# Performance work log

Hardware: AMD Instinct MI355X
Metric: run time of the kernel (lower is better)

Reference implementation:

```python
import jax, jax.numpy as jnp
import numpy as np

N = 50000      # num nodes
EG = 1600000   # num edges (avg degree 32)
IN = 64        # in_dim
OUT = 64       # out_dim
H = 4          # num_heads
D = OUT // H   # per-head dim


def setup_inputs() -> dict:
    key = jax.random.key(0)
    ks = jax.random.split(key, 12)
    s = 1.0 / np.sqrt(IN)
    return {
        "x": jax.random.normal(ks[0], (N, IN), jnp.float32),
        "edge_attr": jax.random.normal(ks[1], (EG, IN), jnp.float32),
        "edge_index": jax.random.randint(ks[2], (2, EG), 0, N, jnp.int32),
        "Wq": jax.random.uniform(ks[3], (OUT, IN), jnp.float32, -s, s),
        "bq": jax.random.uniform(ks[4], (OUT,), jnp.float32, -s, s),
        "Wk": jax.random.uniform(ks[5], (OUT, IN), jnp.float32, -s, s),
        "bk": jax.random.uniform(ks[6], (OUT,), jnp.float32, -s, s),
        "We": jax.random.uniform(ks[7], (OUT, IN), jnp.float32, -s, s),
        "be": jax.random.uniform(ks[8], (OUT,), jnp.float32, -s, s),
        "Wv": jax.random.uniform(ks[9], (OUT, IN), jnp.float32, -s, s),
        "bv": jax.random.uniform(ks[10], (OUT,), jnp.float32, -s, s),
    }


def reference(x, edge_attr, edge_index, Wq, bq, Wk, bk, We, be, Wv, bv):
    n = x.shape[0]
    # linear projections, reshaped to [*, H, D]
    Qh = (x @ Wq.T + bq).reshape(n, H, D)
    Kh = (x @ Wk.T + bk).reshape(n, H, D)
    Vh = (x @ Wv.T + bv).reshape(n, H, D)
    Ee = (edge_attr @ We.T + be).reshape(-1, H, D)
    src = edge_index[0]
    dst = edge_index[1]
    # per-edge score: sum_d K[src] * Q[dst] / sqrt(D) * E  -> [E, H]
    score = ((Kh[src] * Qh[dst]) * (1.0 / np.sqrt(D)) * Ee).sum(-1)
    score = jnp.exp(jnp.clip(score, -5.0, 5.0))            # [E, H]
    msg = Vh[src] * score[..., None]                        # [E, H, D]
    wV = jax.ops.segment_sum(msg, dst, num_segments=n)      # [N, H, D]
    # note: original forward returns wV without dividing by Z
    return wV.reshape(n, H * D)
```

## Files before the change

### kernel.cpp

```cpp
#include <hip/hip_runtime.h>


typedef __attribute__((ext_vector_type(8))) short bf16x8;
typedef __attribute__((ext_vector_type(4))) float f32x4;

union frag_u { uint32_t u[4]; uint4 u4; bf16x8 v; };

__device__ __forceinline__ uint32_t pack2(float a, float b) {
    return (__float_as_uint(a) >> 16) | (__float_as_uint(b) & 0xffff0000u);
}

__device__ __forceinline__ void cvt4(float4 v, uint32_t& h0, uint32_t& h1,
                                     uint32_t& l0, uint32_t& l1) {
    float hx = __uint_as_float(__float_as_uint(v.x) & 0xffff0000u);
    float hy = __uint_as_float(__float_as_uint(v.y) & 0xffff0000u);
    float hz = __uint_as_float(__float_as_uint(v.z) & 0xffff0000u);
    float hw = __uint_as_float(__float_as_uint(v.w) & 0xffff0000u);
    h0 = pack2(v.x, v.y);
    h1 = pack2(v.z, v.w);
    l0 = pack2(v.x - hx, v.y - hy);
    l1 = pack2(v.z - hz, v.w - hw);
}

__global__ __launch_bounds__(256) void proj_kernel(
    const float* __restrict__ x,
    const float* __restrict__ Wq, const float* __restrict__ bq,
    const float* __restrict__ Wk, const float* __restrict__ bk,
    const float* __restrict__ Wv, const float* __restrict__ bv,
    float* __restrict__ Qb, float* __restrict__ KV,
    int n)
{
    __shared__ float WqT[64 * 65];
    __shared__ float WkT[64 * 65];
    __shared__ float WvT[64 * 65];
    __shared__ float xs[4][4][64];

    const int tid  = threadIdx.x;
    const int wave = tid >> 6;
    const int lane = tid & 63;

    #pragma unroll
    for (int k = 0; k < 16; ++k) {
        int idx = tid + k * 256;
        int j = idx >> 6, i = idx & 63;
        WqT[i * 65 + j] = Wq[idx];
        WkT[i * 65 + j] = Wk[idx];
        WvT[i * 65 + j] = Wv[idx];
    }
    const float bqv = bq[lane];
    const float bkv = bk[lane];
    const float bvv = bv[lane];
    __syncthreads();

    for (int blockbase = blockIdx.x * 16; blockbase < n;
         blockbase += gridDim.x * 16) {
        int base = blockbase + wave * 4;
        #pragma unroll
        for (int j = 0; j < 4; ++j) {
            int node = base + j;
            xs[wave][j][lane] = (node < n) ? x[node * 64 + lane] : 0.f;
        }
        __syncthreads();

        float accq[4], acck[4], accv[4];
        #pragma unroll
        for (int j = 0; j < 4; ++j) { accq[j] = bqv; acck[j] = bkv; accv[j] = bvv; }

        #pragma unroll
        for (int f = 0; f < 16; ++f) {
            float wq[4], wk[4], wv[4];
            #pragma unroll
            for (int u = 0; u < 4; ++u) {
                int i = 4 * f + u;
                wq[u] = WqT[i * 65 + lane];
                wk[u] = WkT[i * 65 + lane];
                wv[u] = WvT[i * 65 + lane];
            }
            #pragma unroll
            for (int j = 0; j < 4; ++j) {
                float4 xv = *reinterpret_cast<const float4*>(&xs[wave][j][4 * f]);
                accq[j] = fmaf(xv.x, wq[0], accq[j]);
                accq[j] = fmaf(xv.y, wq[1], accq[j]);
                accq[j] = fmaf(xv.z, wq[2], accq[j]);
                accq[j] = fmaf(xv.w, wq[3], accq[j]);
                acck[j] = fmaf(xv.x, wk[0], acck[j]);
                acck[j] = fmaf(xv.y, wk[1], acck[j]);
                acck[j] = fmaf(xv.z, wk[2], acck[j]);
                acck[j] = fmaf(xv.w, wk[3], acck[j]);
                accv[j] = fmaf(xv.x, wv[0], accv[j]);
                accv[j] = fmaf(xv.y, wv[1], accv[j]);
                accv[j] = fmaf(xv.z, wv[2], accv[j]);
                accv[j] = fmaf(xv.w, wv[3], accv[j]);
            }
        }

        #pragma unroll
        for (int j = 0; j < 4; ++j) {
            int node = base + j;
            if (node < n) {
                Qb[(size_t)node * 64 + lane]       = accq[j];
                KV[(size_t)node * 128 + lane]      = acck[j];
                KV[(size_t)node * 128 + 64 + lane] = accv[j];
            }
        }
        __syncthreads();
    }
}

__global__ __launch_bounds__(256) void edge_kernel(
    const float* __restrict__ ea, const int* __restrict__ ei,
    const float* __restrict__ Qb, const float* __restrict__ KV,
    const float* __restrict__ We, const float* __restrict__ be,
    float* __restrict__ out, int EG)
{
    __shared__ uint4 bfragLDS[16][64];

    const int tid  = threadIdx.x;
    const int wave = __builtin_amdgcn_readfirstlane(tid >> 6);
    const int lane = tid & 63;
    const int g    = lane >> 4;
    const int q    = lane & 15;

    {
        const int nt = wave;
        #pragma unroll
        for (int ks = 0; ks < 2; ++ks) {
            frag_u fh, fl;
            #pragma unroll
            for (int b = 0; b < 2; ++b) {
                float4 w4 = *reinterpret_cast<const float4*>(
                    &We[(size_t)(16 * nt + q) * 64 + 32 * ks + 16 * b + 4 * g]);
                cvt4(w4, fh.u[2 * b + 0], fh.u[2 * b + 1],
                         fl.u[2 * b + 0], fl.u[2 * b + 1]);
            }
            bfragLDS[nt * 4 + ks * 2 + 0][lane] = fh.u4;
            bfragLDS[nt * 4 + ks * 2 + 1][lane] = fl.u4;
        }
    }
    float bias4[4];
    #pragma unroll
    for (int nt = 0; nt < 4; ++nt) bias4[nt] = be[16 * nt + q];
    __syncthreads();

    const int nw  = gridDim.x * 4;
    const int wid = blockIdx.x * 4 + wave;

    for (int eb = wid * 16; eb < EG; eb += nw * 16) {
        int srcs[16], dsts[16];
        #pragma unroll
        for (int r = 0; r < 16; ++r) {
            srcs[r] = ei[eb + r];
            dsts[r] = ei[EG + eb + r];
        }

        frag_u Ah[2], Al[2];
        const float* arow = &ea[(size_t)(eb + q) * 64];
        #pragma unroll
        for (int ks = 0; ks < 2; ++ks) {
            #pragma unroll
            for (int b = 0; b < 2; ++b) {
                float4 a4 = *reinterpret_cast<const float4*>(
                    &arow[32 * ks + 16 * b + 4 * g]);
                cvt4(a4, Ah[ks].u[2 * b + 0], Ah[ks].u[2 * b + 1],
                         Al[ks].u[2 * b + 0], Al[ks].u[2 * b + 1]);
            }
        }

        f32x4 acc[4];
        #pragma unroll
        for (int nt = 0; nt < 4; ++nt) {
            acc[nt][0] = bias4[nt]; acc[nt][1] = bias4[nt];
            acc[nt][2] = bias4[nt]; acc[nt][3] = bias4[nt];
            #pragma unroll
            for (int ks = 0; ks < 2; ++ks) {
                frag_u bh, bl;
                bh.u4 = bfragLDS[nt * 4 + ks * 2 + 0][lane];
                bl.u4 = bfragLDS[nt * 4 + ks * 2 + 1][lane];
                acc[nt] = __builtin_amdgcn_mfma_f32_16x16x32_bf16(
                              Al[ks].v, bh.v, acc[nt], 0, 0, 0);
                acc[nt] = __builtin_amdgcn_mfma_f32_16x16x32_bf16(
                              Ah[ks].v, bl.v, acc[nt], 0, 0, 0);
                acc[nt] = __builtin_amdgcn_mfma_f32_16x16x32_bf16(
                              Ah[ks].v, bh.v, acc[nt], 0, 0, 0);
            }
        }

        #pragma unroll
        for (int r = 0; r < 4; ++r) {
            const int snid = (g & 2) ? ((g & 1) ? srcs[12 + r] : srcs[8 + r])
                                     : ((g & 1) ? srcs[4 + r]  : srcs[r]);
            const int dnid = (g & 2) ? ((g & 1) ? dsts[12 + r] : dsts[8 + r])
                                     : ((g & 1) ? dsts[4 + r]  : dsts[r]);
            const float* kb = KV + (size_t)snid * 128 + q;
            const float* qp = Qb + (size_t)dnid * 64 + q;
            float*       ob = out + (size_t)dnid * 64 + q;

            #pragma unroll
            for (int nt = 0; nt < 4; ++nt) {
                const float kv = kb[16 * nt];
                const float qv = qp[16 * nt];
                float t = kv * qv * 0.25f * acc[nt][r];
                t += __shfl_xor(t, 1);
                t += __shfl_xor(t, 2);
                t += __shfl_xor(t, 4);
                t += __shfl_xor(t, 8);
                t = fminf(fmaxf(t, -5.f), 5.f);
                const float s  = __expf(t);
                const float vv = kb[64 + 16 * nt];
                atomicAdd(&ob[16 * nt], vv * s);
            }
        }
    }
}

extern "C" void kernel_launch(void* const* d_in, const int* in_sizes, int n_in,
                              void* d_out, int out_size, void* d_ws, size_t ws_size,
                              hipStream_t stream) {
    const float* x   = (const float*)d_in[0];
    const float* ea  = (const float*)d_in[1];
    const int*   ei  = (const int*)d_in[2];
    const float* Wq  = (const float*)d_in[3];
    const float* bq  = (const float*)d_in[4];
    const float* Wk  = (const float*)d_in[5];
    const float* bk  = (const float*)d_in[6];
    const float* We  = (const float*)d_in[7];
    const float* be  = (const float*)d_in[8];
    const float* Wv  = (const float*)d_in[9];
    const float* bv  = (const float*)d_in[10];
    float* out = (float*)d_out;

    const int n  = in_sizes[0] / 64;
    const int EG = in_sizes[1] / 64;

    float* Qb = (float*)d_ws;
    float* KV = Qb + (size_t)n * 64;

    hipMemsetAsync(d_out, 0, (size_t)out_size * sizeof(float), stream);

    const int projGrid = (n + 15) / 16;
    proj_kernel<<<projGrid, 256, 0, stream>>>(x, Wq, bq, Wk, bk, Wv, bv,
                                              Qb, KV, n);

    edge_kernel<<<2500, 256, 0, stream>>>(ea, ei, Qb, KV, We, be, out, EG);
}
```

Measured before the change: 546.5 us.

## Replace atomic scatter with CSR-by-destination aggregation via count, scan, permute

Builds a destination-sorted CSR (degree histogram fused into the projection kernel, three-pass scan, atomic scatter into a permutation) and then aggregates per destination node in registers, writing each output row once. This removes the 64 float atomics per edge and the output memset, and keeps Q per destination in registers. In exchange it adds several small kernels, integer atomics for counting and scattering, and indirect gathers of edge_attr rows through the permutation. It also relies on n divisible by 4 and EG divisible by 4, and the single-block scanB limits the node count to 65536, which covers this n.

New measurement: 531.5 us. 2.7% less time.

```diff
diff --git a/kernel.cpp b/kernel.cpp
--- a/kernel.cpp
+++ b/kernel.cpp
@@ -3,13 +3,11 @@
 
 typedef __attribute__((ext_vector_type(8))) short bf16x8;
 typedef __attribute__((ext_vector_type(4))) float f32x4;
-
 union frag_u { uint32_t u[4]; uint4 u4; bf16x8 v; };
 
 __device__ __forceinline__ uint32_t pack2(float a, float b) {
     return (__float_as_uint(a) >> 16) | (__float_as_uint(b) & 0xffff0000u);
 }
-
 __device__ __forceinline__ void cvt4(float4 v, uint32_t& h0, uint32_t& h1,
                                      uint32_t& l0, uint32_t& l1) {
     float hx = __uint_as_float(__float_as_uint(v.x) & 0xffff0000u);
@@ -27,8 +25,9 @@
     const float* __restrict__ Wq, const float* __restrict__ bq,
     const float* __restrict__ Wk, const float* __restrict__ bk,
     const float* __restrict__ Wv, const float* __restrict__ bv,
+    const int* __restrict__ ei, int* __restrict__ cnt,
     float* __restrict__ Qb, float* __restrict__ KV,
-    int n)
+    int n, int EG)
 {
     __shared__ float WqT[64 * 65];
     __shared__ float WkT[64 * 65];
@@ -105,15 +104,94 @@
         }
         __syncthreads();
     }
-}
-
-__global__ __launch_bounds__(256) void edge_kernel(
+
+    {
+        const int nt4 = EG >> 2;
+        int i  = blockIdx.x * blockDim.x + threadIdx.x;
+        int st = gridDim.x * blockDim.x;
+        const int4* d4 = reinterpret_cast<const int4*>(ei + EG);
+        for (int e = i; e < nt4; e += st) {
+            int4 d = d4[e];
+            atomicAdd(&cnt[d.x], 1);
+            atomicAdd(&cnt[d.y], 1);
+            atomicAdd(&cnt[d.z], 1);
+            atomicAdd(&cnt[d.w], 1);
+        }
+    }
+}
+
+__global__ __launch_bounds__(256) void scanA_kernel(
+    const int* __restrict__ cnt, int* __restrict__ off,
+    int* __restrict__ bsum, int n)
+{
+    __shared__ int s[256];
+    const int t = threadIdx.x;
+    const int i = blockIdx.x * 256 + t;
+    const int v = (i < n) ? cnt[i] : 0;
+    s[t] = v;
+    __syncthreads();
+    for (int d = 1; d < 256; d <<= 1) {
+        int u = (t >= d) ? s[t - d] : 0;
+        __syncthreads();
+        s[t] += u;
+        __syncthreads();
+    }
+    if (i < n) off[i] = s[t] - v;
+    if (t == 255) bsum[blockIdx.x] = s[255];
+}
+
+__global__ __launch_bounds__(256) void scanB_kernel(int* __restrict__ bsum, int nb)
+{
+    __shared__ int s[256];
+    const int t = threadIdx.x;
+    const int v = (t < nb) ? bsum[t] : 0;
+    s[t] = v;
+    __syncthreads();
+    for (int d = 1; d < 256; d <<= 1) {
+        int u = (t >= d) ? s[t - d] : 0;
+        __syncthreads();
+        s[t] += u;
+        __syncthreads();
+    }
+    if (t < nb) bsum[t] = s[t] - v;
+}
+
+__global__ __launch_bounds__(256) void scanC_kernel(
+    int* __restrict__ off, const int* __restrict__ bsum,
+    int* __restrict__ cursor, int n, int EG)
+{
+    const int i = blockIdx.x * 256 + threadIdx.x;
+    if (i < n) {
+        int v = off[i] + bsum[blockIdx.x];
+        off[i] = v;
+        cursor[i] = v;
+    }
+    if (i == 0) off[n] = EG;
+}
+
+__global__ __launch_bounds__(256) void scatter_kernel(
+    const int* __restrict__ ei, int* __restrict__ cursor,
+    int* __restrict__ perm, int EG)
+{
+    int i  = blockIdx.x * blockDim.x + threadIdx.x;
+    int st = gridDim.x * blockDim.x;
+    for (int e = i; e < EG; e += st) {
+        int d = ei[EG + e];
+        int p = atomicAdd(&cursor[d], 1);
+        perm[p] = e;
+    }
+}
+
+__global__ __launch_bounds__(256) void agg_kernel(
     const float* __restrict__ ea, const int* __restrict__ ei,
+    const int* __restrict__ off, const int* __restrict__ perm,
     const float* __restrict__ Qb, const float* __restrict__ KV,
     const float* __restrict__ We, const float* __restrict__ be,
-    float* __restrict__ out, int EG)
+    float* __restrict__ out, int n, int EG)
 {
     __shared__ uint4 bfragLDS[16][64];
+    __shared__ int sidt[4][16];
+    __shared__ int eidt[4][16];
 
     const int tid  = threadIdx.x;
     const int wave = __builtin_amdgcn_readfirstlane(tid >> 6);
@@ -143,73 +221,99 @@
     __syncthreads();
 
     const int nw  = gridDim.x * 4;
-    const int wid = blockIdx.x * 4 + wave;
-
-    for (int eb = wid * 16; eb < EG; eb += nw * 16) {
-        int srcs[16], dsts[16];
-        #pragma unroll
-        for (int r = 0; r < 16; ++r) {
-            srcs[r] = ei[eb + r];
-            dsts[r] = ei[EG + eb + r];
-        }
-
-        frag_u Ah[2], Al[2];
-        const float* arow = &ea[(size_t)(eb + q) * 64];
-        #pragma unroll
-        for (int ks = 0; ks < 2; ++ks) {
-            #pragma unroll
-            for (int b = 0; b < 2; ++b) {
-                float4 a4 = *reinterpret_cast<const float4*>(
-                    &arow[32 * ks + 16 * b + 4 * g]);
-                cvt4(a4, Ah[ks].u[2 * b + 0], Ah[ks].u[2 * b + 1],
-                         Al[ks].u[2 * b + 0], Al[ks].u[2 * b + 1]);
-            }
-        }
-
-        f32x4 acc[4];
-        #pragma unroll
-        for (int nt = 0; nt < 4; ++nt) {
-            acc[nt][0] = bias4[nt]; acc[nt][1] = bias4[nt];
-            acc[nt][2] = bias4[nt]; acc[nt][3] = bias4[nt];
+    const int nd4 = n >> 2;
+
+    for (int wid = blockIdx.x * 4 + wave; wid < nd4; wid += nw) {
+        const int dbase = wid << 2;
+        const int mydst = dbase + g;
+        const int j0  = off[mydst];
+        const int j1  = off[mydst + 1];
+        const int deg = j1 - j0;
+
+        float qreg[4];
+        #pragma unroll
+        for (int nt = 0; nt < 4; ++nt)
+            qreg[nt] = Qb[(size_t)mydst * 64 + 16 * nt + q];
+
+        const int grp  = (lane & 15) >> 2;
+        const int slot = lane & 3;
+        const int j0p  = __shfl(j0, grp << 4);
+        const int j1p  = __shfl(j1, grp << 4);
+
+        int dm = max(deg, __shfl_xor(deg, 16));
+        dm = max(dm, __shfl_xor(dm, 32));
+        const int iters = __builtin_amdgcn_readfirstlane((dm + 3) >> 2);
+
+        float macc[4] = {0.f, 0.f, 0.f, 0.f};
+
+        for (int c = 0; c < iters; ++c) {
+            if (lane < 16) {
+                const int  p     = j0p + 4 * c + slot;
+                const bool valid = p < j1p;
+                const int  eid   = valid ? perm[p] : 0;
+                const int  src   = valid ? ei[eid] : -1;
+                eidt[wave][lane] = eid;
+                sidt[wave][lane] = src;
+            }
+            __builtin_amdgcn_wave_barrier();
+
+            const int eidq = eidt[wave][q];
+            const float* arow = ea + (size_t)eidq * 64;
+            frag_u Ah[2], Al[2];
             #pragma unroll
             for (int ks = 0; ks < 2; ++ks) {
-                frag_u bh, bl;
-                bh.u4 = bfragLDS[nt * 4 + ks * 2 + 0][lane];
-                bl.u4 = bfragLDS[nt * 4 + ks * 2 + 1][lane];
-                acc[nt] = __builtin_amdgcn_mfma_f32_16x16x32_bf16(
-                              Al[ks].v, bh.v, acc[nt], 0, 0, 0);
-                acc[nt] = __builtin_amdgcn_mfma_f32_16x16x32_bf16(
-                              Ah[ks].v, bl.v, acc[nt], 0, 0, 0);
-                acc[nt] = __builtin_amdgcn_mfma_f32_16x16x32_bf16(
-                              Ah[ks].v, bh.v, acc[nt], 0, 0, 0);
-            }
-        }
-
-        #pragma unroll
-        for (int r = 0; r < 4; ++r) {
-            const int snid = (g & 2) ? ((g & 1) ? srcs[12 + r] : srcs[8 + r])
-                                     : ((g & 1) ? srcs[4 + r]  : srcs[r]);
-            const int dnid = (g & 2) ? ((g & 1) ? dsts[12 + r] : dsts[8 + r])
-                                     : ((g & 1) ? dsts[4 + r]  : dsts[r]);
-            const float* kb = KV + (size_t)snid * 128 + q;
-            const float* qp = Qb + (size_t)dnid * 64 + q;
-            float*       ob = out + (size_t)dnid * 64 + q;
-
+                #pragma unroll
+                for (int b = 0; b < 2; ++b) {
+                    float4 a4 = *reinterpret_cast<const float4*>(
+                        &arow[32 * ks + 16 * b + 4 * g]);
+                    cvt4(a4, Ah[ks].u[2 * b + 0], Ah[ks].u[2 * b + 1],
+                             Al[ks].u[2 * b + 0], Al[ks].u[2 * b + 1]);
+                }
+            }
+
+            f32x4 acc[4];
             #pragma unroll
             for (int nt = 0; nt < 4; ++nt) {
-                const float kv = kb[16 * nt];
-                const float qv = qp[16 * nt];
-                float t = kv * qv * 0.25f * acc[nt][r];
-                t += __shfl_xor(t, 1);
-                t += __shfl_xor(t, 2);
-                t += __shfl_xor(t, 4);
-                t += __shfl_xor(t, 8);
-                t = fminf(fmaxf(t, -5.f), 5.f);
-                const float s  = __expf(t);
-                const float vv = kb[64 + 16 * nt];
-                atomicAdd(&ob[16 * nt], vv * s);
-            }
-        }
+                acc[nt][0] = bias4[nt]; acc[nt][1] = bias4[nt];
+                acc[nt][2] = bias4[nt]; acc[nt][3] = bias4[nt];
+                #pragma unroll
+                for (int ks = 0; ks < 2; ++ks) {
+                    frag_u bh, bl;
+                    bh.u4 = bfragLDS[nt * 4 + ks * 2 + 0][lane];
+                    bl.u4 = bfragLDS[nt * 4 + ks * 2 + 1][lane];
+                    acc[nt] = __builtin_amdgcn_mfma_f32_16x16x32_bf16(
+                                  Al[ks].v, bh.v, acc[nt], 0, 0, 0);
+                    acc[nt] = __builtin_amdgcn_mfma_f32_16x16x32_bf16(
+                                  Ah[ks].v, bl.v, acc[nt], 0, 0, 0);
+                    acc[nt] = __builtin_amdgcn_mfma_f32_16x16x32_bf16(
+                                  Ah[ks].v, bh.v, acc[nt], 0, 0, 0);
+                }
+            }
+
+            #pragma unroll
+            for (int r = 0; r < 4; ++r) {
+                const int srcr = sidt[wave][4 * g + r];
+                const float* kb = KV + (size_t)(srcr < 0 ? 0 : srcr) * 128 + q;
+                #pragma unroll
+                for (int nt = 0; nt < 4; ++nt) {
+                    const float kv = kb[16 * nt];
+                    const float vv = kb[64 + 16 * nt];
+                    float t = kv * qreg[nt] * 0.25f * acc[nt][r];
+                    t += __shfl_xor(t, 1);
+                    t += __shfl_xor(t, 2);
+                    t += __shfl_xor(t, 4);
+                    t += __shfl_xor(t, 8);
+                    t = fminf(fmaxf(t, -5.f), 5.f);
+                    const float s = __expf(t);
+                    if (srcr >= 0) macc[nt] = fmaf(vv, s, macc[nt]);
+                }
+            }
+            __builtin_amdgcn_wave_barrier();
+        }
+
+        #pragma unroll
+        for (int nt = 0; nt < 4; ++nt)
+            out[(size_t)mydst * 64 + 16 * nt + q] = macc[nt];
     }
 }
 
@@ -232,14 +336,28 @@
     const int n  = in_sizes[0] / 64;
     const int EG = in_sizes[1] / 64;
 
-    float* Qb = (float*)d_ws;
-    float* KV = Qb + (size_t)n * 64;
-
-    hipMemsetAsync(d_out, 0, (size_t)out_size * sizeof(float), stream);
+    float* Qb   = (float*)d_ws;
+    float* KV   = Qb + (size_t)n * 64;
+    int* cnt    = (int*)(KV + (size_t)n * 128);
+    int* off    = cnt + n;
+    int* cursor = off + n + 1;
+    int* perm   = cursor + n;
+    int* bsum   = perm + EG;
+
+    hipMemsetAsync(cnt, 0, (size_t)n * sizeof(int), stream);
 
     const int projGrid = (n + 15) / 16;
     proj_kernel<<<projGrid, 256, 0, stream>>>(x, Wq, bq, Wk, bk, Wv, bv,
-                                              Qb, KV, n);
-
-    edge_kernel<<<2500, 256, 0, stream>>>(ea, ei, Qb, KV, We, be, out, EG);
-}
+                                              ei, cnt, Qb, KV, n, EG);
+
+    const int nb = (n + 255) / 256;
+    scanA_kernel<<<nb, 256, 0, stream>>>(cnt, off, bsum, n);
+    scanB_kernel<<<1, 256, 0, stream>>>(bsum, nb);
+    scanC_kernel<<<nb, 256, 0, stream>>>(off, bsum, cursor, n, EG);
+
+    scatter_kernel<<<2048, 256, 0, stream>>>(ei, cursor, perm, EG);
+
+    const int aggGrid = (n / 4 + 3) / 4;
+    agg_kernel<<<aggGrid, 256, 0, stream>>>(ea, ei, off, perm,
+                                            Qb, KV, We, be, out, n, EG);
+}
```
